# Performance work log

Measured on AMD Instinct MI355X. Metric: run time of the kernel, lower is better.

## Reference

```python
import jax, jax.numpy as jnp
import numpy as np

C = 64
K = 3          # kernel_size
EK = 5         # encoder_kernel
PAD = (K - 1) // 2


def _conv(x, w, pad):
    return jax.lax.conv_general_dilated(
        x, w, window_strides=(1, 1), padding=[(pad, pad), (pad, pad)],
        dimension_numbers=('NCHW', 'OIHW', 'NCHW'))


def setup_inputs() -> dict:
    key = jax.random.key(0)
    ks = jax.random.split(key, 6)
    b, h, w = 8, 128, 128
    x = jax.random.normal(ks[0], (b, C, h, w), dtype=jnp.float32)
    # gen_kernel: 1x1 conv (C->C, with bias) then EKxEK conv (C->K*K, no bias)
    w1 = jax.random.normal(ks[1], (C, C, 1, 1), dtype=jnp.float32) * (1.0 / np.sqrt(C))
    b1 = jax.random.normal(ks[2], (C,), dtype=jnp.float32) * 0.01
    w2 = jax.random.normal(ks[3], (K * K, C, EK, EK), dtype=jnp.float32) * (1.0 / np.sqrt(C * EK * EK))
    # consensus t_c: 1x1 conv C->C//4, relu, 1x1 conv C//4->C, relu (no bias)
    tc1 = jax.random.normal(ks[4], (C // 4, C, 1, 1), dtype=jnp.float32) * (1.0 / np.sqrt(C))
    tc2 = jax.random.normal(ks[5], (C, C // 4, 1, 1), dtype=jnp.float32) * (1.0 / np.sqrt(C // 4))
    return {"x": x, "w1": w1, "b1": b1, "w2": w2, "tc1": tc1, "tc2": tc2}


def reference(x, w1, b1, w2, tc1, tc2):
    b, c, h, w = x.shape
    oh, ow = h, w  # stride == 1
    # dynamic kernel logits: (b, K*K, oh, ow)
    y = _conv(x, w1, 0) + b1[None, :, None, None]
    wt = _conv(y, w2, (EK - 1) // 2)
    # consensus scale: adaptive avg pool to 1x1 then mean over batch -> (c,)
    x_con = jnp.mean(x, axis=(0, 2, 3))                      # (c,)
    h1 = jax.nn.relu(jnp.einsum('oc,c->o', tc1[:, :, 0, 0], x_con))
    tmp = jax.nn.relu(jnp.einsum('oc,c->o', tc2[:, :, 0, 0], h1))  # (c,)
    # broadcast logits to (b, c, K*K, oh, ow) and softmax over K*K
    logits = wt[:, None, :, :, :] * tmp[None, :, None, None, None]
    attn = jax.nn.softmax(logits, axis=2)                    # (b,c,9,oh,ow)
    # unfold patches: reflect-pad then 9 shifted views, order kh*K+kw (row-major)
    px = jnp.pad(x, ((0, 0), (0, 0), (PAD, PAD), (PAD, PAD)), mode='reflect')
    pats = jnp.stack([px[:, :, i:i + oh, j:j + ow]
                      for i in range(K) for j in range(K)], axis=2)  # (b,c,9,oh,ow)
    out = jnp.sum(attn * pats, axis=2)                       # (b,c,oh,ow)
    return out
```

## Files before the change

kernel.cpp:

```cpp
#include <hip/hip_runtime.h>
#include <hip/hip_bf16.h>
#include <cstddef>


#define B 8
#define C 64
#define HW 128
#define NK 9
#define NT 25
#define XR 132
#define TI 8
#define TJ 16
#define HR 12
#define HC 20
#define LOG2E 1.4426950408889634f

typedef __attribute__((ext_vector_type(8))) short short8;
typedef __attribute__((ext_vector_type(4))) float float4v;
typedef __attribute__((ext_vector_type(4))) unsigned int uint4v;

__device__ __forceinline__ unsigned short f2bf(float f) {
    unsigned int u = __float_as_uint(f);
    unsigned int r = u + 0x7FFF + ((u >> 16) & 1);
    return (unsigned short)(r >> 16);
}
__device__ __forceinline__ float fast_exp2(float x) {
    float r;
    asm("v_exp_f32 %0, %1" : "=v"(r) : "v"(x));
    return r;
}
__device__ __forceinline__ float fast_rcp(float x) {
    float r;
    asm("v_rcp_f32 %0, %1" : "=v"(r) : "v"(x));
    return r;
}
__device__ __forceinline__ void load_lds16(const unsigned short* g, unsigned short* l) {
    __builtin_amdgcn_global_load_lds(
        (const __attribute__((address_space(1))) unsigned int*)g,
        (__attribute__((address_space(3))) unsigned int*)l,
        16, 0, 0);
}

__global__ __launch_bounds__(256) void xpack_kernel(const float* __restrict__ x,
                                                    unsigned short* __restrict__ xbf,
                                                    float* __restrict__ part_rows) {
    const int r = blockIdx.x, b = blockIdx.y;
    unsigned short* rowp = xbf + ((size_t)(b * XR + r)) * (XR * 64);
    const int t = threadIdx.x;
    if (r < 2 || r >= 130) {
        const uint4v z = {0u, 0u, 0u, 0u};
        for (int idx = t; idx < 1056; idx += 256)
            *(uint4v*)(rowp + idx * 8) = z;
        return;
    }
    const int h = r - 2;
    if (t < 32) {
        const uint4v z = {0u, 0u, 0u, 0u};
        const int q4 = t & 3;
        const int wc = (q4 < 2) ? q4 : (q4 + 128);
        *(uint4v*)(rowp + wc * 64 + ((t >> 2) << 3)) = z;
    }
    const int c8 = t >> 5;
    const int wl = t & 31;
    const float* xp = x + (((size_t)(b * C + c8 * 8)) * HW + h) * HW;
    float s8[8] = {0.f, 0.f, 0.f, 0.f, 0.f, 0.f, 0.f, 0.f};
#pragma unroll
    for (int k = 0; k < 4; ++k) {
        const int gw = wl + 32 * k;
        const int wc = gw + 2;
        uint4v dv;
#pragma unroll
        for (int j = 0; j < 4; ++j) {
            const float v0 = xp[(size_t)(2 * j) * (HW * HW) + gw];
            const float v1 = xp[(size_t)(2 * j + 1) * (HW * HW) + gw];
            s8[2 * j] += v0;
            s8[2 * j + 1] += v1;
            dv[j] = (unsigned int)f2bf(v0) | ((unsigned int)f2bf(v1) << 16);
        }
        const int sw = ((r & 1) * 4 + wc) & 7;
        *(uint4v*)(rowp + wc * 64 + ((c8 ^ sw) << 3)) = dv;
    }
#pragma unroll
    for (int off = 16; off > 0; off >>= 1) {
#pragma unroll
        for (int j = 0; j < 8; ++j) s8[j] += __shfl_down(s8[j], off);
    }
    if (wl == 0) {
        float* pr = part_rows + ((size_t)(b * HW + h)) * 64 + c8 * 8;
#pragma unroll
        for (int j = 0; j < 8; ++j) pr[j] = s8[j];
    }
}

__global__ __launch_bounds__(256) void prep_kernel(const float* __restrict__ w1,
                                                   const float* __restrict__ b1,
                                                   const float* __restrict__ w2,
                                                   const float* __restrict__ part_rows,
                                                   unsigned short* __restrict__ Abuf,
                                                   float* __restrict__ betaG,
                                                   float* __restrict__ part) {
    if (blockIdx.x < 50) {
        __shared__ float sw2[NK * 64];
        __shared__ float sw1[64 * 32];
        const int chunk = blockIdx.x;
        const int t = chunk >> 1, ch = chunk & 1;
        for (int idx = threadIdx.x; idx < NK * 64; idx += 256) {
            const int m = idx >> 6, cc = idx & 63;
            sw2[idx] = w2[(m * 64 + cc) * NT + t];
        }
        for (int idx = threadIdx.x; idx < 2048; idx += 256) {
            const int cc = idx >> 5, j = idx & 31;
            sw1[idx] = w1[cc * 64 + ch * 32 + j];
        }
        __syncthreads();
        for (int sidx = 0; sidx < 2; ++sidx) {
            const int slot = sidx * 256 + threadIdx.x;
            const int quad = slot >> 7, m = (slot >> 3) & 15, jj = slot & 7;
            unsigned short hi = 0, lo = 0;
            if (m < NK) {
                float s = 0.f;
                for (int cc = 0; cc < 64; ++cc)
                    s += sw2[m * 64 + cc] * sw1[cc * 32 + quad * 8 + jj];
                hi = f2bf(s);
                lo = f2bf(s - __uint_as_float(((unsigned int)hi) << 16));
            }
            Abuf[chunk * 1024 + slot] = hi;
            Abuf[chunk * 1024 + 512 + slot] = lo;
        }
    } else if (blockIdx.x == 50) {
        __shared__ float beta_s[NT * NK];
        const int t0 = threadIdx.x;
        if (t0 < NT * NK) {
            const int t = t0 / NK, k = t0 - t * NK;
            float s = 0.f;
            for (int cc = 0; cc < 64; ++cc)
                s += w2[(k * 64 + cc) * NT + t] * b1[cc];
            beta_s[t0] = s;
        }
        __syncthreads();
        if (t0 < 225) {
            const int ic = t0 / 45, jc = (t0 / 9) % 5, k = t0 % 9;
            float s = 0.f;
            for (int eh = 0; eh < 5; ++eh) {
                bool rok = (ic == 0) ? (eh >= 2) : (ic == 1) ? (eh >= 1)
                          : (ic == 3) ? (eh <= 3) : (ic == 4) ? (eh <= 2) : true;
                if (!rok) continue;
                for (int ew = 0; ew < 5; ++ew) {
                    bool cok = (jc == 0) ? (ew >= 2) : (jc == 1) ? (ew >= 1)
                              : (jc == 3) ? (ew <= 3) : (jc == 4) ? (ew <= 2) : true;
                    if (cok) s += beta_s[(eh * 5 + ew) * NK + k];
                }
            }
            betaG[t0] = s;
        }
    } else {
        const int c = threadIdx.x >> 2, seg = threadIdx.x & 3;
        const float* pr = part_rows + (size_t)(seg * 256) * 64 + c;
        float s0 = 0.f, s1 = 0.f, s2 = 0.f, s3 = 0.f;
#pragma unroll 4
        for (int i = 0; i < 256; i += 4) {
            s0 += pr[(size_t)(i + 0) * 64];
            s1 += pr[(size_t)(i + 1) * 64];
            s2 += pr[(size_t)(i + 2) * 64];
            s3 += pr[(size_t)(i + 3) * 64];
        }
        part[c * 4 + seg] = (s0 + s1) + (s2 + s3);
    }
}

__global__ __launch_bounds__(256, 4) void fused_kernel(const unsigned short* __restrict__ xbf,
                                                       const unsigned short* __restrict__ Abuf,
                                                       const float* __restrict__ betaG,
                                                       const float* __restrict__ part,
                                                       const float* __restrict__ tc1,
                                                       const float* __restrict__ tc2,
                                                       float* __restrict__ out) {
    __shared__ __align__(16) unsigned short stag[HR * HC * 64];
    __shared__ float wpart[128 * 9];
    __shared__ float lt[C];
    const int b = blockIdx.y;
    const int i0 = (blockIdx.x >> 3) * TI, j0 = (blockIdx.x & 7) * TJ;
    const int tid = threadIdx.x, lane = tid & 63, wid = tid >> 6;
    const int n = lane & 15, q = lane >> 4;
    const int rowg = wid >> 1, h = wid & 1;

    {
        const unsigned short* xrow0 = xbf + (((size_t)(b * XR + i0)) * XR + j0) * 64;
#pragma unroll
        for (int k = 0; k < 7; ++k) {
            const int ci = k * 256 + tid;
            const int li = ((ci >> 5) * 205) >> 10;
            const int rem = ci - li * 160;
            load_lds16(xrow0 + li * (XR * 64) + rem * 8, stag + ci * 8);
        }
        if (tid < 128) {
            const int ci = 1792 + tid;
            const int li = ((ci >> 5) * 205) >> 10;
            const int rem = ci - li * 160;
            load_lds16(xrow0 + li * (XR * 64) + rem * 8, stag + ci * 8);
        }
    }

    if (wid == 0) {
        float xcv = (part[lane * 4 + 0] + part[lane * 4 + 1]
                   + part[lane * 4 + 2] + part[lane * 4 + 3]) * (1.f / (B * HW * HW));
        float hh = 0.f;
        for (int c = 0; c < C; ++c) {
            float xcc = __shfl(xcv, c);
            if (lane < 16) hh += tc1[lane * C + c] * xcc;
        }
        hh = fmaxf(hh, 0.f);
        float ltv = 0.f;
#pragma unroll
        for (int o = 0; o < 16; ++o) {
            float ho = __shfl(hh, o);
            ltv += tc2[lane * 16 + o] * ho;
        }
        lt[lane] = fmaxf(ltv, 0.f) * LOG2E;
    }

    const int prow = rowg * 4 + q;
    const int pgi = i0 + prow, pgj = j0 + n;
    float bgv[NK];
    if (h == 0) {
        const int ic = pgi < 2 ? pgi : (pgi > 125 ? pgi - 123 : 2);
        const int jc = pgj < 2 ? pgj : (pgj > 125 ? pgj - 123 : 2);
        const float* bp = betaG + (ic * 5 + jc) * NK;
#pragma unroll
        for (int k = 0; k < NK; ++k) bgv[k] = bp[k];
    }

    __syncthreads();

    float4v acc[4];
    const float4v zero4 = {0.f, 0.f, 0.f, 0.f};
#pragma unroll
    for (int g = 0; g < 4; ++g) acc[g] = zero4;

    const unsigned short* Ab = Abuf + h * 1024 + lane * 8;
    const int chs = (h << 2) | q;
    const int rb = rowg * 4;
#pragma unroll
    for (int ew = 0; ew < 5; ++ew) {
        short8 w8[8];
#pragma unroll
        for (int rr = 0; rr < 8; ++rr) {
            const int px = (rb + rr) * HC + ew + n;
            w8[rr] = *(const short8*)(stag + px * 64 + ((chs ^ (px & 7)) << 3));
        }
#pragma unroll
        for (int eh = 0; eh < 5; ++eh) {
            const int t = eh * 5 + ew;
            const short8 ahi = *(const short8*)(Ab + t * 2048);
            const short8 alo = *(const short8*)(Ab + t * 2048 + 512);
#pragma unroll
            for (int g = 0; g < 4; ++g) {
                acc[g] = __builtin_amdgcn_mfma_f32_16x16x32_bf16(ahi, w8[g + eh], acc[g], 0, 0, 0);
                acc[g] = __builtin_amdgcn_mfma_f32_16x16x32_bf16(alo, w8[g + eh], acc[g], 0, 0, 0);
            }
        }
    }

    float wv[NK];
#pragma unroll
    for (int k = 0; k < NK; ++k) {
        const int src = (k >> 2) * 16 + n;
        const int rr = k & 3;
        float v0 = __shfl(acc[0][rr], src);
        float v1 = __shfl(acc[1][rr], src);
        float v2 = __shfl(acc[2][rr], src);
        float v3 = __shfl(acc[3][rr], src);
        wv[k] = (q == 0) ? v0 : (q == 1) ? v1 : (q == 2) ? v2 : v3;
    }

    const int slot = rowg * 64 + lane;
    if (h == 1) {
#pragma unroll
        for (int k = 0; k < NK; ++k) wpart[slot * 9 + k] = wv[k];
    }
    __syncthreads();
    if (h == 0) {
        float w9[NK];
        float wmax = -1e30f;
#pragma unroll
        for (int k = 0; k < NK; ++k) {
            w9[k] = wv[k] + wpart[slot * 9 + k] + bgv[k];
            wmax = fmaxf(wmax, w9[k]);
        }
#pragma unroll
        for (int k = 0; k < NK; ++k) wpart[slot * 9 + k] = w9[k] - wmax;
    }
    __syncthreads();

#pragma unroll
    for (int sp = 0; sp < 2; ++sp) {
        const int lpx = lane + (sp << 6);
        const int brow = lpx >> 4, bcol = lpx & 15;
        const int bgi = i0 + brow, bgj = j0 + bcol;
        float dv[NK];
#pragma unroll
        for (int k = 0; k < NK; ++k) dv[k] = wpart[lpx * 9 + k];
        int r0 = bgi - 1; r0 = r0 < 0 ? 1 : r0;
        int r2 = bgi + 1; r2 = r2 > 127 ? 126 : r2;
        int c0 = bgj - 1; c0 = c0 < 0 ? 1 : c0;
        int c2 = bgj + 1; c2 = c2 > 127 ? 126 : c2;
        const int R[3] = {r0 - i0 + 2, bgi - i0 + 2, r2 - i0 + 2};
        const int Cc[3] = {c0 - j0 + 2, bgj - j0 + 2, c2 - j0 + 2};
#pragma unroll
        for (int oc = 0; oc < 2; ++oc) {
            const int oct = wid * 2 + oc;
            uint4v xs[NK];
#pragma unroll
            for (int kh = 0; kh < 3; ++kh)
#pragma unroll
                for (int kw = 0; kw < 3; ++kw) {
                    const int prc = R[kh] * HC + Cc[kw];
                    xs[kh * 3 + kw] = *(const uint4v*)(stag + prc * 64 + ((oct ^ (prc & 7)) << 3));
                }
            float* outp = out + (((size_t)b * C + oct * 8) * HW + bgi) * HW + bgj;
#pragma unroll
            for (int jj = 0; jj < 4; ++jj) {
                const float t0 = lt[oct * 8 + jj * 2];
                const float t1 = lt[oct * 8 + jj * 2 + 1];
                float s0 = 0.f, o0 = 0.f, s1 = 0.f, o1 = 0.f;
#pragma unroll
                for (int k = 0; k < NK; ++k) {
                    const unsigned int u = xs[k][jj];
                    const float e0 = fast_exp2(dv[k] * t0);
                    const float e1 = fast_exp2(dv[k] * t1);
                    s0 += e0; o0 = fmaf(e0, __uint_as_float(u << 16), o0);
                    s1 += e1; o1 = fmaf(e1, __uint_as_float(u & 0xffff0000u), o1);
                }
                outp[(size_t)(jj * 2) * (HW * HW)] = o0 * fast_rcp(s0);
                outp[(size_t)(jj * 2 + 1) * (HW * HW)] = o1 * fast_rcp(s1);
            }
        }
    }
}

extern "C" void kernel_launch(void* const* d_in, const int* in_sizes, int n_in,
                              void* d_out, int out_size, void* d_ws, size_t ws_size,
                              hipStream_t stream) {
    const float* x   = (const float*)d_in[0];
    const float* w1  = (const float*)d_in[1];
    const float* b1  = (const float*)d_in[2];
    const float* w2  = (const float*)d_in[3];
    const float* tc1 = (const float*)d_in[4];
    const float* tc2 = (const float*)d_in[5];
    float* out = (float*)d_out;

    char* ws = (char*)d_ws;
    float* part  = (float*)(ws + 0);
    unsigned short* Abuf = (unsigned short*)(ws + 1024);
    float* betaG = (float*)(ws + 103424);
    float* part_rows = (float*)(ws + 104448);
    unsigned short* xbf  = (unsigned short*)(ws + 366592);

    xpack_kernel<<<dim3(XR, B), 256, 0, stream>>>(x, xbf, part_rows);
    prep_kernel<<<52, 256, 0, stream>>>(w1, b1, w2, part_rows, Abuf, betaG, part);
    fused_kernel<<<dim3(128, B), 256, 0, stream>>>(xbf, Abuf, betaG, part, tc1, tc2, out);
}
```

Measured before the change: 132.1 us.

## Hoist consensus MLP into prep kernel and drop softmax max-reduction barrier

```diff
diff --git a/kernel.cpp b/kernel.cpp
--- a/kernel.cpp
+++ b/kernel.cpp
@@ -96,9 +96,11 @@
                                                    const float* __restrict__ b1,
                                                    const float* __restrict__ w2,
                                                    const float* __restrict__ part_rows,
+                                                   const float* __restrict__ tc1,
+                                                   const float* __restrict__ tc2,
                                                    unsigned short* __restrict__ Abuf,
                                                    float* __restrict__ betaG,
-                                                   float* __restrict__ part) {
+                                                   float* __restrict__ ltg) {
     if (blockIdx.x < 50) {
         __shared__ float sw2[NK * 64];
         __shared__ float sw1[64 * 32];
@@ -154,6 +156,7 @@
             betaG[t0] = s;
         }
     } else {
+        __shared__ float pl[256];
         const int c = threadIdx.x >> 2, seg = threadIdx.x & 3;
         const float* pr = part_rows + (size_t)(seg * 256) * 64 + c;
         float s0 = 0.f, s1 = 0.f, s2 = 0.f, s3 = 0.f;
@@ -164,20 +167,37 @@
             s2 += pr[(size_t)(i + 2) * 64];
             s3 += pr[(size_t)(i + 3) * 64];
         }
-        part[c * 4 + seg] = (s0 + s1) + (s2 + s3);
+        pl[threadIdx.x] = (s0 + s1) + (s2 + s3);
+        __syncthreads();
+        if (threadIdx.x < 64) {
+            const int lane = threadIdx.x;
+            float xcv = (pl[lane * 4 + 0] + pl[lane * 4 + 1]
+                       + pl[lane * 4 + 2] + pl[lane * 4 + 3]) * (1.f / (B * HW * HW));
+            float hh = 0.f;
+            for (int c2 = 0; c2 < C; ++c2) {
+                float xcc = __shfl(xcv, c2);
+                if (lane < 16) hh += tc1[lane * C + c2] * xcc;
+            }
+            hh = fmaxf(hh, 0.f);
+            float ltv = 0.f;
+#pragma unroll
+            for (int o = 0; o < 16; ++o) {
+                float ho = __shfl(hh, o);
+                ltv += tc2[lane * 16 + o] * ho;
+            }
+            ltg[lane] = fmaxf(ltv, 0.f) * LOG2E;
+        }
     }
 }
 
 __global__ __launch_bounds__(256, 4) void fused_kernel(const unsigned short* __restrict__ xbf,
                                                        const unsigned short* __restrict__ Abuf,
                                                        const float* __restrict__ betaG,
-                                                       const float* __restrict__ part,
-                                                       const float* __restrict__ tc1,
-                                                       const float* __restrict__ tc2,
+                                                       const float* __restrict__ ltg,
                                                        float* __restrict__ out) {
     __shared__ __align__(16) unsigned short stag[HR * HC * 64];
-    __shared__ float wpart[128 * 9];
-    __shared__ float lt[C];
+    __shared__ float wpA[NK * 128];
+    __shared__ float wpB[NK * 128];
     const int b = blockIdx.y;
     const int i0 = (blockIdx.x >> 3) * TI, j0 = (blockIdx.x & 7) * TJ;
     const int tid = threadIdx.x, lane = tid & 63, wid = tid >> 6;
@@ -199,24 +219,6 @@
             const int rem = ci - li * 160;
             load_lds16(xrow0 + li * (XR * 64) + rem * 8, stag + ci * 8);
         }
-    }
-
-    if (wid == 0) {
-        float xcv = (part[lane * 4 + 0] + part[lane * 4 + 1]
-                   + part[lane * 4 + 2] + part[lane * 4 + 3]) * (1.f / (B * HW * HW));
-        float hh = 0.f;
-        for (int c = 0; c < C; ++c) {
-            float xcc = __shfl(xcv, c);
-            if (lane < 16) hh += tc1[lane * C + c] * xcc;
-        }
-        hh = fmaxf(hh, 0.f);
-        float ltv = 0.f;
-#pragma unroll
-        for (int o = 0; o < 16; ++o) {
-            float ho = __shfl(hh, o);
-            ltv += tc2[lane * 16 + o] * ho;
-        }
-        lt[lane] = fmaxf(ltv, 0.f) * LOG2E;
     }
 
     const int prow = rowg * 4 + q;
@@ -274,21 +276,12 @@
     }
 
     const int slot = rowg * 64 + lane;
-    if (h == 1) {
-#pragma unroll
-        for (int k = 0; k < NK; ++k) wpart[slot * 9 + k] = wv[k];
-    }
-    __syncthreads();
     if (h == 0) {
-        float w9[NK];
-        float wmax = -1e30f;
-#pragma unroll
-        for (int k = 0; k < NK; ++k) {
-            w9[k] = wv[k] + wpart[slot * 9 + k] + bgv[k];
-            wmax = fmaxf(wmax, w9[k]);
-        }
-#pragma unroll
-        for (int k = 0; k < NK; ++k) wpart[slot * 9 + k] = w9[k] - wmax;
+#pragma unroll
+        for (int k = 0; k < NK; ++k) wpA[k * 128 + slot] = wv[k] + bgv[k];
+    } else {
+#pragma unroll
+        for (int k = 0; k < NK; ++k) wpB[k * 128 + slot] = wv[k];
     }
     __syncthreads();
 
@@ -299,7 +292,7 @@
         const int bgi = i0 + brow, bgj = j0 + bcol;
         float dv[NK];
 #pragma unroll
-        for (int k = 0; k < NK; ++k) dv[k] = wpart[lpx * 9 + k];
+        for (int k = 0; k < NK; ++k) dv[k] = wpA[k * 128 + lpx] + wpB[k * 128 + lpx];
         int r0 = bgi - 1; r0 = r0 < 0 ? 1 : r0;
         int r2 = bgi + 1; r2 = r2 > 127 ? 126 : r2;
         int c0 = bgj - 1; c0 = c0 < 0 ? 1 : c0;
@@ -320,8 +313,8 @@
             float* outp = out + (((size_t)b * C + oct * 8) * HW + bgi) * HW + bgj;
 #pragma unroll
             for (int jj = 0; jj < 4; ++jj) {
-                const float t0 = lt[oct * 8 + jj * 2];
-                const float t1 = lt[oct * 8 + jj * 2 + 1];
+                const float t0 = ltg[oct * 8 + jj * 2];
+                const float t1 = ltg[oct * 8 + jj * 2 + 1];
                 float s0 = 0.f, o0 = 0.f, s1 = 0.f, o1 = 0.f;
 #pragma unroll
                 for (int k = 0; k < NK; ++k) {
@@ -350,13 +343,13 @@
     float* out = (float*)d_out;
 
     char* ws = (char*)d_ws;
-    float* part  = (float*)(ws + 0);
+    float* ltg   = (float*)(ws + 0);
     unsigned short* Abuf = (unsigned short*)(ws + 1024);
     float* betaG = (float*)(ws + 103424);
     float* part_rows = (float*)(ws + 104448);
     unsigned short* xbf  = (unsigned short*)(ws + 366592);
 
     xpack_kernel<<<dim3(XR, B), 256, 0, stream>>>(x, xbf, part_rows);
-    prep_kernel<<<52, 256, 0, stream>>>(w1, b1, w2, part_rows, Abuf, betaG, part);
-    fused_kernel<<<dim3(128, B), 256, 0, stream>>>(xbf, Abuf, betaG, part, tc1, tc2, out);
-}
+    prep_kernel<<<52, 256, 0, stream>>>(w1, b1, w2, part_rows, tc1, tc2, Abuf, betaG, ltg);
+    fused_kernel<<<dim3(128, B), 256, 0, stream>>>(xbf, Abuf, betaG, ltg, out);
+}
```

Result: no change. 132.1 us (+0.0%).
